# Kernel optimization log

Hardware: AMD Instinct MI355X
Metric: run time of the kernel (lower is better)

The kernel has to match this reference:

```python
import jax, jax.numpy as jnp
import numpy as np

B, N, S, DG, C_IN, C_OUT, HID = 2, 128, 4, 8, 4, 8, 32


def setup_inputs() -> dict:
    key = jax.random.key(0)
    ks = jax.random.split(key, 10)

    def w(k, shape, fan_in):
        return jax.random.normal(k, shape, jnp.float32) / np.float32(np.sqrt(fan_in))

    return {
        "pairwise_g": jax.random.normal(ks[0], (B, N, N, S, S, DG), jnp.float32),
        "coset_functions": jax.random.normal(ks[1], (B, N, S, C_IN), jnp.float32),
        "mask": jax.random.bernoulli(ks[2], 0.9, (B, N, S)),
        "ky_W1": w(ks[3], (C_IN, HID, 2), 2), "ky_b1": jnp.zeros((C_IN, HID), jnp.float32),
        "ky_W2": w(ks[4], (C_IN, HID, HID), HID), "ky_b2": jnp.zeros((C_IN, HID), jnp.float32),
        "ky_W3": w(ks[5], (C_IN, 1, HID), HID), "ky_b3": jnp.zeros((C_IN, 1), jnp.float32),
        "kg_W1": w(ks[6], (C_IN, HID, DG), DG), "kg_b1": jnp.zeros((C_IN, HID), jnp.float32),
        "kg_W2": w(ks[7], (C_IN, HID, HID), HID), "kg_b2": jnp.zeros((C_IN, HID), jnp.float32),
        "kg_W3": w(ks[8], (C_IN, 1, HID), HID), "kg_b3": jnp.zeros((C_IN, 1), jnp.float32),
        "w_out": w(ks[9], (C_OUT, C_IN), C_IN),
    }


def _mlp(x, W1, b1, W2, b2, W3, b3):
    # NerualNetKernel with bn=False, act=Swish: (Linear + SiLU) x 3, incl. output layer.
    h = jax.nn.silu(x @ W1.T + b1)
    h = jax.nn.silu(h @ W2.T + b2)
    return jax.nn.silu(h @ W3.T + b3)


def reference(pairwise_g, coset_functions, mask,
              ky_W1, ky_b1, ky_W2, ky_b2, ky_W3, ky_b3,
              kg_W1, kg_b1, kg_W2, kg_b2, kg_W3, kg_b3, w_out):
    b, n, _, s, _, _ = pairwise_g.shape
    c_in = coset_functions.shape[-1]
    key_mask = mask[:, None, :, None, :, None]  # (B,1,N,1,S,1) masks key points/samples
    outs = []
    for i in range(c_in):  # fixed small channel loop, as in the original module
        f = coset_functions[..., i:i + 1]  # (B,N,S,1)
        y1 = jnp.broadcast_to(f[:, None, :, None, :, :], (b, n, n, s, s, 1))  # key side
        y2 = jnp.broadcast_to(f[:, :, None, :, None, :], (b, n, n, s, s, 1))  # query side
        y = jnp.concatenate([y1, y2], axis=-1)  # (B,N,N,S,S,2)
        k = (_mlp(y, ky_W1[i], ky_b1[i], ky_W2[i], ky_b2[i], ky_W3[i], ky_b3[i])
             + _mlp(pairwise_g, kg_W1[i], kg_b1[i], kg_W2[i], kg_b2[i], kg_W3[i], kg_b3[i]))
        att = jnp.where(key_mask, jnp.exp(k), jnp.zeros((), k.dtype))  # (B,N,N,S,S,1)
        att = att / att.sum(axis=(2, 4), keepdims=True)
        f = f + (att * f[:, None, :, None, :, :]).sum(axis=(2, 4))  # residual + weighted agg
        outs.append(f)
    cf = jnp.concatenate(outs, axis=-1)  # (B,N,S,C_IN)
    cf = cf * mask[..., None].astype(cf.dtype)
    return cf @ w_out.T  # (B,N,S,C_OUT), bias-free output transform
```

## Files before the change

kernel.cpp:

```cpp
#include <hip/hip_runtime.h>
#include <hip/hip_bf16.h>

#define BB   2
#define NN   128
#define SS   4
#define DGG  8
#define CIN  4
#define COUT 8
#define HH   32
#define NT   256

typedef __attribute__((ext_vector_type(4))) float          fvec4;
typedef __attribute__((ext_vector_type(4))) unsigned short usvec4;
typedef __attribute__((ext_vector_type(8))) unsigned short usvec8;
typedef __attribute__((ext_vector_type(2))) __fp16         half2v;
typedef __attribute__((ext_vector_type(8))) __fp16         f16x8;
typedef __attribute__((ext_vector_type(4))) float          f32x4;
typedef __attribute__((ext_vector_type(4))) unsigned int   uvec4;

__device__ __forceinline__ float bf2f(unsigned short u) {
    return __uint_as_float(((unsigned int)u) << 16);
}
__device__ __forceinline__ float silu_f(float x) {
    float e = __builtin_amdgcn_exp2f(x * -1.44269504f);
    return x * __builtin_amdgcn_rcpf(1.0f + e);
}
__device__ __forceinline__ float exp_f(float x) {
    return __builtin_amdgcn_exp2f(x * 1.44269504f);
}

__device__ __forceinline__ unsigned int pk2u(float a, float b) {
#if __has_builtin(__builtin_amdgcn_cvt_pkrtz)
    half2v h = __builtin_amdgcn_cvt_pkrtz(a, b);
#else
    half2v h; h[0] = (__fp16)a; h[1] = (__fp16)b;
#endif
    union { half2v h; unsigned int u; } x; x.h = h; return x.u;
}
union FU { uvec4 u; f16x8 h; };
__device__ __forceinline__ f16x8 mk_frag(unsigned a, unsigned b, unsigned c, unsigned d) {
    FU x; x.u = (uvec4){a, b, c, d}; return x.h;
}
__device__ __forceinline__ f16x8 mk_fragv(uvec4 u) {
    FU x; x.u = u; return x.h;
}
__device__ __forceinline__ f16x8 silu_frag(f32x4 a, f32x4 b) {
    return mk_frag(pk2u(silu_f(a[0]), silu_f(a[1])),
                   pk2u(silu_f(a[2]), silu_f(a[3])),
                   pk2u(silu_f(b[0]), silu_f(b[1])),
                   pk2u(silu_f(b[2]), silu_f(b[3])));
}

__device__ __forceinline__ float loadS(const void* p, int idx, int fmode) {
    return fmode ? bf2f(((const unsigned short*)p)[idx])
                 : ((const float*)p)[idx];
}
__device__ __forceinline__ void load8(const void* p, int base, int fmode, float* dst) {
    if (fmode) {
        usvec8 v = *(const usvec8*)((const unsigned short*)p + base);
#pragma unroll
        for (int d = 0; d < 8; ++d) dst[d] = bf2f(v[d]);
    } else {
        fvec4 a = *(const fvec4*)((const float*)p + base);
        fvec4 b = *(const fvec4*)((const float*)p + base + 4);
        dst[0] = a[0]; dst[1] = a[1]; dst[2] = a[2]; dst[3] = a[3];
        dst[4] = b[0]; dst[5] = b[1]; dst[6] = b[2]; dst[7] = b[3];
    }
}
__device__ __forceinline__ int load_mask(const void* p, int idx, int mmode) {
    if (mmode == 0) return ((const int*)p)[idx] != 0;
    if (mmode == 1) return ((const unsigned short*)p)[idx] != 0;
    if (mmode == 2) return ((const unsigned char*)p)[idx] != 0;
    return ((const unsigned int*)p)[idx] != 0;
}
__device__ __forceinline__ void stage_pk(unsigned int* dst, const void* src,
                                         int pairs, int fmode, int tid) {
    if (fmode) {
        const unsigned short* s = (const unsigned short*)src;
        for (int x = tid; x < pairs; x += NT)
            dst[x] = pk2u(bf2f(s[2 * x]), bf2f(s[2 * x + 1]));
    } else {
        const float* s = (const float*)src;
        for (int x = tid; x < pairs; x += NT)
            dst[x] = pk2u(s[2 * x], s[2 * x + 1]);
    }
}
__device__ __forceinline__ void copy_arr(float* sm, const void* src, int off,
                                         int cnt, int fmode, int tid) {
    if (fmode) {
        const unsigned short* s = (const unsigned short*)src;
        for (int x = tid; x < cnt; x += NT) sm[off + x] = bf2f(s[x]);
    } else {
        const float* s = (const float*)src;
        for (int x = tid; x < cnt; x += NT) sm[off + x] = s[x];
    }
}
__device__ __forceinline__ void detect_inline(const void* g_mask, const void* g_coset,
                                              int tid, int* smi, int slot) {
    if (tid < 64) {
        const unsigned short* cu = (const unsigned short*)g_coset;
        unsigned short v = cu[2 * tid];
        int e = (v >> 7) & 0xFF;
        int hits = __popcll(__ballot(e >= 110 && e <= 135));
        int fmode_ = (hits > 32) ? 1 : 0;
        const unsigned short* mu = (const unsigned short*)g_mask;
        int evenBF = 0, any3 = 0, anyByte = 0;
        for (int r = 0; r < 8; ++r) {
            int idx = tid + r * 64;
            unsigned short m = mu[idx];
            if (m == 0x3F80) { any3 = 1; if (!(idx & 1)) evenBF = 1; }
            if (m == 0x0101 || m == 0x0100) anyByte = 1;
        }
        evenBF  = (__ballot(evenBF)  != 0ull);
        any3    = (__ballot(any3)    != 0ull);
        anyByte = (__ballot(anyByte) != 0ull);
        if (tid == 0) {
            smi[slot]     = fmode_;
            smi[slot + 1] = evenBF ? 1 : (any3 ? 3 : (anyByte ? 2 : 0));
        }
    }
}

#define UG_G    0
#define F_FA    2048
#define U_YW1n  4096
#define U_GW1   4608
#define U_GB1q  5120
#define U_W2Y   5632
#define U_W2G   7680
#define F_YB2   9728
#define F_GB2   9856
#define U_YW3   9984
#define U_GW3   10048
#define F_YB3   10112
#define F_GB3   10116
#define U_CB1   10120
#define F_RED   10128
#define F_MODE  10160
#define U_TOTAL 10162

__global__ __launch_bounds__(NT, 4) void emha_mfma(
    const void* __restrict__ g_pw, const void* __restrict__ g_coset,
    const void* __restrict__ g_mask,
    const void* yW1, const void* yb1, const void* yW2, const void* yb2,
    const void* yW3, const void* yb3,
    const void* gW1, const void* gb1, const void* gW2, const void* gb2,
    const void* gW3, const void* gb3,
    const void* wout, void* outp)
{
    __shared__ __align__(16) unsigned int smu[U_TOTAL];
    float* smf = (float*)smu;
    int*   smi = (int*)smu;
    const int tid = threadIdx.x;

    detect_inline(g_mask, g_coset, tid, smi, F_MODE);
    __syncthreads();
    const int fmode = smi[F_MODE];
    const int mmode = smi[F_MODE + 1];
    __syncthreads();

    const int bn = blockIdx.x >> 2;
    const int s1 = blockIdx.x & 3;
    const int b  = bn >> 7;
    const int n1 = bn & 127;

#pragma unroll
    for (int it = 0; it < 2; ++it) {
        const int pos = tid + it * 256;
        const int n2 = pos >> 2, s2 = pos & 3;
        float g8[8];
        load8(g_pw, (((bn * NN + n2) * SS + s1) * SS + s2) * DGG, fmode, g8);
#pragma unroll
        for (int q = 0; q < 4; ++q)
            smu[UG_G + pos * 4 + q] = pk2u(g8[2 * q], g8[2 * q + 1]);
    }
    for (int x = tid; x < 2048; x += NT)
        smf[F_FA + x] = loadS(g_coset, b * 2048 + x, fmode);
    for (int x = tid; x < 128; x += NT) {
        smu[U_YW1n + x * 4 + 0] = pk2u(loadS(yW1, 2 * x, fmode), loadS(yW1, 2 * x + 1, fmode));
        smu[U_YW1n + x * 4 + 1] = pk2u(loadS(yb1, x, fmode), 0.f);
        smu[U_YW1n + x * 4 + 2] = 0u;
        smu[U_YW1n + x * 4 + 3] = 0u;
        smu[U_GB1q + x * 4 + 0] = pk2u(loadS(gb1, x, fmode), 0.f);
        smu[U_GB1q + x * 4 + 1] = 0u;
        smu[U_GB1q + x * 4 + 2] = 0u;
        smu[U_GB1q + x * 4 + 3] = 0u;
    }
    stage_pk(&smu[U_GW1], gW1, 512,  fmode, tid);
    stage_pk(&smu[U_W2Y], yW2, 2048, fmode, tid);
    stage_pk(&smu[U_W2G], gW2, 2048, fmode, tid);
    stage_pk(&smu[U_YW3], yW3, 64,   fmode, tid);
    stage_pk(&smu[U_GW3], gW3, 64,   fmode, tid);
    copy_arr(smf, yb2, F_YB2, 128, fmode, tid);
    copy_arr(smf, gb2, F_GB2, 128, fmode, tid);
    copy_arr(smf, yb3, F_YB3, 4, fmode, tid);
    copy_arr(smf, gb3, F_GB3, 4, fmode, tid);
    if (tid < 8) smu[U_CB1 + tid] = (tid == 0) ? 0x00003C00u : 0u;

    const int lane = tid & 63;
    const int wave = tid >> 6;
    const int mLo = load_mask(g_mask, b * 512 + wave * 128 + lane, mmode);
    const int mHi = load_mask(g_mask, b * 512 + wave * 128 + 64 + lane, mmode);
    const unsigned long long kmL = __ballot(mLo != 0);
    const unsigned long long kmH = __ballot(mHi != 0);
    __syncthreads();

    const int quad = lane >> 4;
    const int col  = lane & 15;
    const int qpos = n1 * 4 + s1;
    const int h0   = ((col >> 2) << 3) + (col & 3);
    const unsigned* Zp = &smu[U_CB1 + 4];
    const f32x4 zf = {0.f, 0.f, 0.f, 0.f};

#pragma unroll 1
    for (int ci = 0; ci < CIN; ++ci) {
        const int rowy = (ci * 32 + h0) * 4;
        const f16x8 AY1a = mk_fragv(*(const uvec4*)((quad == 0) ? &smu[U_YW1n + rowy] : Zp));
        const f16x8 AY1b = mk_fragv(*(const uvec4*)((quad == 0) ? &smu[U_YW1n + rowy + 16] : Zp));
        const f16x8 GA = mk_fragv(*(const uvec4*)((quad == 0) ? &smu[U_GW1 + rowy]
                                   : (quad == 1) ? &smu[U_GB1q + rowy] : Zp));
        const f16x8 GB = mk_fragv(*(const uvec4*)((quad == 0) ? &smu[U_GW1 + rowy + 16]
                                   : (quad == 1) ? &smu[U_GB1q + rowy + 16] : Zp));
        const f16x8 Ay0 = mk_fragv(*(const uvec4*)&smu[U_W2Y + ci * 512 + h0 * 16 + quad * 4]);
        const f16x8 Ay1 = mk_fragv(*(const uvec4*)&smu[U_W2Y + ci * 512 + (h0 + 4) * 16 + quad * 4]);
        const f16x8 Ag0 = mk_fragv(*(const uvec4*)&smu[U_W2G + ci * 512 + h0 * 16 + quad * 4]);
        const f16x8 Ag1 = mk_fragv(*(const uvec4*)&smu[U_W2G + ci * 512 + (h0 + 4) * 16 + quad * 4]);
        const fvec4 cY0 = *(const fvec4*)&smf[F_YB2 + ci * 32 + quad * 8];
        const fvec4 cY1 = *(const fvec4*)&smf[F_YB2 + ci * 32 + quad * 8 + 4];
        const fvec4 cG0 = *(const fvec4*)&smf[F_GB2 + ci * 32 + quad * 8];
        const fvec4 cG1 = *(const fvec4*)&smf[F_GB2 + ci * 32 + quad * 8 + 4];
        const f16x8 A3y = mk_fragv(*(const uvec4*)((col == 0) ? &smu[U_YW3 + ci * 16 + quad * 4] : Zp));
        const f16x8 A3g = mk_fragv(*(const uvec4*)((col == 0) ? &smu[U_GW3 + ci * 16 + quad * 4] : Zp));

        const float fb  = smf[F_FA + qpos * 4 + ci];
        const float b3y = smf[F_YB3 + ci];
        const float b3g = smf[F_GB3 + ci];

        const unsigned* pBg = (quad == 0) ? &smu[UG_G + (wave * 128 + col) * 4]
                            : ((quad == 1) ? &smu[U_CB1] : Zp);
        const int stepBg = (quad == 0) ? 64 : 0;
        const float* pFA = &smf[F_FA + (wave * 128 + col) * 4 + ci];

        float aN = 0.f, aD = 0.f;
#pragma unroll 2
        for (int t = 0; t < 8; ++t) {
            const uvec4 gq = *(const uvec4*)pBg;
            const float fap = *pFA;
            const f16x8 Bg1 = mk_fragv(gq);
            const f16x8 B1y = mk_frag(pk2u(fap, fb), 0x00003C00u, 0u, 0u);

            f32x4 d1a, d1b, dga, dgb, dy0, dy1, dg0, dg1, dy3, dg3;
#if defined(__HIP_DEVICE_COMPILE__)
            d1a = __builtin_amdgcn_mfma_f32_16x16x32_f16(AY1a, B1y, zf, 0, 0, 0);
            d1b = __builtin_amdgcn_mfma_f32_16x16x32_f16(AY1b, B1y, zf, 0, 0, 0);
            dga = __builtin_amdgcn_mfma_f32_16x16x32_f16(GA,   Bg1, zf, 0, 0, 0);
            dgb = __builtin_amdgcn_mfma_f32_16x16x32_f16(GB,   Bg1, zf, 0, 0, 0);
#else
            d1a = zf; d1b = zf; dga = zf; dgb = zf;
#endif
            const f16x8 By = silu_frag(d1a, d1b);
            const f16x8 Bg = silu_frag(dga, dgb);

#if defined(__HIP_DEVICE_COMPILE__)
            dy0 = __builtin_amdgcn_mfma_f32_16x16x32_f16(Ay0, By, cY0, 0, 0, 0);
            dy1 = __builtin_amdgcn_mfma_f32_16x16x32_f16(Ay1, By, cY1, 0, 0, 0);
            dg0 = __builtin_amdgcn_mfma_f32_16x16x32_f16(Ag0, Bg, cG0, 0, 0, 0);
            dg1 = __builtin_amdgcn_mfma_f32_16x16x32_f16(Ag1, Bg, cG1, 0, 0, 0);
#else
            dy0 = cY0; dy1 = cY1; dg0 = cG0; dg1 = cG1;
#endif
            const f16x8 By2 = silu_frag(dy0, dy1);
            const f16x8 Bg2 = silu_frag(dg0, dg1);

#if defined(__HIP_DEVICE_COMPILE__)
            dy3 = __builtin_amdgcn_mfma_f32_16x16x32_f16(A3y, By2, zf, 0, 0, 0);
            dg3 = __builtin_amdgcn_mfma_f32_16x16x32_f16(A3g, Bg2, zf, 0, 0, 0);
#else
            dy3 = zf; dg3 = zf;
#endif
            const float kyv = silu_f(dy3[0] + b3y);
            const float kgv = silu_f(dg3[0] + b3g);
            const unsigned long long sel = (t < 4) ? kmL : kmH;
            const int kb = (int)((sel >> (((t & 3) << 4) + col)) & 1);
            const float e = kb ? exp_f(kyv + kgv) : 0.f;
            aD += e;
            aN += e * fap;

            pBg += stepBg;
            pFA += 64;
        }
        aN += __shfl_xor(aN, 1);  aD += __shfl_xor(aD, 1);
        aN += __shfl_xor(aN, 2);  aD += __shfl_xor(aD, 2);
        aN += __shfl_xor(aN, 4);  aD += __shfl_xor(aD, 4);
        aN += __shfl_xor(aN, 8);  aD += __shfl_xor(aD, 8);
        if (lane == 0) {
            smf[F_RED + (wave * 4 + ci) * 2 + 0] = aN;
            smf[F_RED + (wave * 4 + ci) * 2 + 1] = aD;
        }
    }
    __syncthreads();

    if (tid < COUT) {
        const int o = tid;
        const int m1 = load_mask(g_mask, b * 512 + qpos, mmode);
        float acc = 0.f;
#pragma unroll
        for (int ci = 0; ci < CIN; ++ci) {
            float N = 0.f, D = 0.f;
#pragma unroll
            for (int w = 0; w < 4; ++w) {
                N += smf[F_RED + (w * 4 + ci) * 2 + 0];
                D += smf[F_RED + (w * 4 + ci) * 2 + 1];
            }
            const float fbv = smf[F_FA + qpos * 4 + ci];
            const float cf = m1 ? (fbv + N / D) : 0.f;
            acc += cf * loadS(wout, o * CIN + ci, fmode);
        }
        const int oidx = (bn * SS + s1) * COUT + o;
        if (fmode) ((__hip_bfloat16*)outp)[oidx] = __float2bfloat16(acc);
        else       ((float*)outp)[oidx] = acc;
    }
}

extern "C" void kernel_launch(void* const* d_in, const int* in_sizes, int n_in,
                              void* d_out, int out_size, void* d_ws, size_t ws_size,
                              hipStream_t stream) {
    emha_mfma<<<BB * NN * SS, NT, 0, stream>>>(
        d_in[0], d_in[1], d_in[2],
        d_in[3], d_in[4], d_in[5], d_in[6], d_in[7], d_in[8],
        d_in[9], d_in[10], d_in[11], d_in[12], d_in[13], d_in[14],
        d_in[15], d_out);
}
```

Measured before the change: 168.9 us.

## Use six waves per block with strided tile assignment and smem mask bytes

Raises the block from 4 to 6 waves and distributes the 32 key tiles round-robin across waves (6 iterations with a bounds check) instead of a fixed 8 tiles per wave. The key mask is staged into shared memory as bytes, replacing per-wave ballots, and the layer-1 weight buffers are compacted so zero fragments are built in registers instead of read from padded LDS. The intent is more latency hiding per CU from extra waves. The cost is load imbalance (two waves do 6 tiles, four do 5), a divergent branch inside the loop, and a larger block that may cut blocks per CU.

Measured after the change: 208.7 us. +23.5%, slower.

```diff
diff --git a/kernel.cpp b/kernel.cpp
--- a/kernel.cpp
+++ b/kernel.cpp
@@ -8,7 +8,8 @@
 #define CIN  4
 #define COUT 8
 #define HH   32
-#define NT   256
+#define NT   384
+#define NW   6
 
 typedef __attribute__((ext_vector_type(4))) float          fvec4;
 typedef __attribute__((ext_vector_type(4))) unsigned short usvec4;
@@ -123,23 +124,24 @@
 
 #define UG_G    0
 #define F_FA    2048
-#define U_YW1n  4096
-#define U_GW1   4608
-#define U_GB1q  5120
-#define U_W2Y   5632
-#define U_W2G   7680
-#define F_YB2   9728
-#define F_GB2   9856
-#define U_YW3   9984
-#define U_GW3   10048
-#define F_YB3   10112
-#define F_GB3   10116
-#define U_CB1   10120
-#define F_RED   10128
-#define F_MODE  10160
-#define U_TOTAL 10162
-
-__global__ __launch_bounds__(NT, 4) void emha_mfma(
+#define U_MASKB 4096
+#define U_YW1c  4224
+#define U_GW1   4480
+#define U_GB1c  4992
+#define U_W2Y   5120
+#define U_W2G   7168
+#define F_YB2   9216
+#define F_GB2   9344
+#define U_YW3   9472
+#define U_GW3   9536
+#define F_YB3   9600
+#define F_GB3   9604
+#define U_CB1   9608
+#define F_RED   9616
+#define F_MODE  9664
+#define U_TOTAL 9666
+
+__global__ __launch_bounds__(NT, NW) void emha_mfma(
     const void* __restrict__ g_pw, const void* __restrict__ g_coset,
     const void* __restrict__ g_mask,
     const void* yW1, const void* yb1, const void* yW2, const void* yb2,
@@ -164,9 +166,7 @@
     const int b  = bn >> 7;
     const int n1 = bn & 127;
 
-#pragma unroll
-    for (int it = 0; it < 2; ++it) {
-        const int pos = tid + it * 256;
+    for (int pos = tid; pos < 512; pos += NT) {
         const int n2 = pos >> 2, s2 = pos & 3;
         float g8[8];
         load8(g_pw, (((bn * NN + n2) * SS + s1) * SS + s2) * DGG, fmode, g8);
@@ -176,15 +176,15 @@
     }
     for (int x = tid; x < 2048; x += NT)
         smf[F_FA + x] = loadS(g_coset, b * 2048 + x, fmode);
+    {
+        unsigned char* mbs = (unsigned char*)&smu[U_MASKB];
+        for (int x = tid; x < 512; x += NT)
+            mbs[x] = (unsigned char)load_mask(g_mask, b * 512 + x, mmode);
+    }
     for (int x = tid; x < 128; x += NT) {
-        smu[U_YW1n + x * 4 + 0] = pk2u(loadS(yW1, 2 * x, fmode), loadS(yW1, 2 * x + 1, fmode));
-        smu[U_YW1n + x * 4 + 1] = pk2u(loadS(yb1, x, fmode), 0.f);
-        smu[U_YW1n + x * 4 + 2] = 0u;
-        smu[U_YW1n + x * 4 + 3] = 0u;
-        smu[U_GB1q + x * 4 + 0] = pk2u(loadS(gb1, x, fmode), 0.f);
-        smu[U_GB1q + x * 4 + 1] = 0u;
-        smu[U_GB1q + x * 4 + 2] = 0u;
-        smu[U_GB1q + x * 4 + 3] = 0u;
+        smu[U_YW1c + x * 2 + 0] = pk2u(loadS(yW1, 2 * x, fmode), loadS(yW1, 2 * x + 1, fmode));
+        smu[U_YW1c + x * 2 + 1] = pk2u(loadS(yb1, x, fmode), 0.f);
+        smu[U_GB1c + x]         = pk2u(loadS(gb1, x, fmode), 0.f);
     }
     stage_pk(&smu[U_GW1], gW1, 512,  fmode, tid);
     stage_pk(&smu[U_W2Y], yW2, 2048, fmode, tid);
@@ -196,31 +196,35 @@
     copy_arr(smf, yb3, F_YB3, 4, fmode, tid);
     copy_arr(smf, gb3, F_GB3, 4, fmode, tid);
     if (tid < 8) smu[U_CB1 + tid] = (tid == 0) ? 0x00003C00u : 0u;
+    __syncthreads();
 
     const int lane = tid & 63;
     const int wave = tid >> 6;
-    const int mLo = load_mask(g_mask, b * 512 + wave * 128 + lane, mmode);
-    const int mHi = load_mask(g_mask, b * 512 + wave * 128 + 64 + lane, mmode);
-    const unsigned long long kmL = __ballot(mLo != 0);
-    const unsigned long long kmH = __ballot(mHi != 0);
-    __syncthreads();
-
     const int quad = lane >> 4;
     const int col  = lane & 15;
     const int qpos = n1 * 4 + s1;
     const int h0   = ((col >> 2) << 3) + (col & 3);
-    const unsigned* Zp = &smu[U_CB1 + 4];
+    const unsigned char* mb = (const unsigned char*)&smu[U_MASKB];
     const f32x4 zf = {0.f, 0.f, 0.f, 0.f};
+    const uvec4 zz = {0u, 0u, 0u, 0u};
 
 #pragma unroll 1
     for (int ci = 0; ci < CIN; ++ci) {
-        const int rowy = (ci * 32 + h0) * 4;
-        const f16x8 AY1a = mk_fragv(*(const uvec4*)((quad == 0) ? &smu[U_YW1n + rowy] : Zp));
-        const f16x8 AY1b = mk_fragv(*(const uvec4*)((quad == 0) ? &smu[U_YW1n + rowy + 16] : Zp));
-        const f16x8 GA = mk_fragv(*(const uvec4*)((quad == 0) ? &smu[U_GW1 + rowy]
-                                   : (quad == 1) ? &smu[U_GB1q + rowy] : Zp));
-        const f16x8 GB = mk_fragv(*(const uvec4*)((quad == 0) ? &smu[U_GW1 + rowy + 16]
-                                   : (quad == 1) ? &smu[U_GB1q + rowy + 16] : Zp));
+        const int rw = ci * 32 + h0;
+        uvec4 va = zz, vb = zz, ga = zz, gb = zz;
+        if (quad == 0) {
+            va[0] = smu[U_YW1c + rw * 2];       va[1] = smu[U_YW1c + rw * 2 + 1];
+            vb[0] = smu[U_YW1c + (rw + 4) * 2]; vb[1] = smu[U_YW1c + (rw + 4) * 2 + 1];
+            ga = *(const uvec4*)&smu[U_GW1 + rw * 4];
+            gb = *(const uvec4*)&smu[U_GW1 + (rw + 4) * 4];
+        } else if (quad == 1) {
+            ga[0] = smu[U_GB1c + rw];
+            gb[0] = smu[U_GB1c + rw + 4];
+        }
+        const f16x8 AY1a = mk_fragv(va);
+        const f16x8 AY1b = mk_fragv(vb);
+        const f16x8 GA   = mk_fragv(ga);
+        const f16x8 GB   = mk_fragv(gb);
         const f16x8 Ay0 = mk_fragv(*(const uvec4*)&smu[U_W2Y + ci * 512 + h0 * 16 + quad * 4]);
         const f16x8 Ay1 = mk_fragv(*(const uvec4*)&smu[U_W2Y + ci * 512 + (h0 + 4) * 16 + quad * 4]);
         const f16x8 Ag0 = mk_fragv(*(const uvec4*)&smu[U_W2G + ci * 512 + h0 * 16 + quad * 4]);
@@ -229,65 +233,62 @@
         const fvec4 cY1 = *(const fvec4*)&smf[F_YB2 + ci * 32 + quad * 8 + 4];
         const fvec4 cG0 = *(const fvec4*)&smf[F_GB2 + ci * 32 + quad * 8];
         const fvec4 cG1 = *(const fvec4*)&smf[F_GB2 + ci * 32 + quad * 8 + 4];
-        const f16x8 A3y = mk_fragv(*(const uvec4*)((col == 0) ? &smu[U_YW3 + ci * 16 + quad * 4] : Zp));
-        const f16x8 A3g = mk_fragv(*(const uvec4*)((col == 0) ? &smu[U_GW3 + ci * 16 + quad * 4] : Zp));
+        const f16x8 A3y = mk_fragv((col == 0) ? *(const uvec4*)&smu[U_YW3 + ci * 16 + quad * 4] : zz);
+        const f16x8 A3g = mk_fragv((col == 0) ? *(const uvec4*)&smu[U_GW3 + ci * 16 + quad * 4] : zz);
 
         const float fb  = smf[F_FA + qpos * 4 + ci];
         const float b3y = smf[F_YB3 + ci];
         const float b3g = smf[F_GB3 + ci];
 
-        const unsigned* pBg = (quad == 0) ? &smu[UG_G + (wave * 128 + col) * 4]
-                            : ((quad == 1) ? &smu[U_CB1] : Zp);
-        const int stepBg = (quad == 0) ? 64 : 0;
-        const float* pFA = &smf[F_FA + (wave * 128 + col) * 4 + ci];
-
         float aN = 0.f, aD = 0.f;
-#pragma unroll 2
-        for (int t = 0; t < 8; ++t) {
-            const uvec4 gq = *(const uvec4*)pBg;
-            const float fap = *pFA;
-            const f16x8 Bg1 = mk_fragv(gq);
-            const f16x8 B1y = mk_frag(pk2u(fap, fb), 0x00003C00u, 0u, 0u);
-
-            f32x4 d1a, d1b, dga, dgb, dy0, dy1, dg0, dg1, dy3, dg3;
+#pragma unroll 1
+        for (int t = 0; t < 6; ++t) {
+            const int tile = t * NW + wave;
+            if (tile < 32) {
+                const int pos = tile * 16 + col;
+                const float fap = smf[F_FA + pos * 4 + ci];
+                const int km = mb[pos];
+                uvec4 gq;
+                if (quad == 0) gq = *(const uvec4*)&smu[UG_G + pos * 4];
+                else           gq = (uvec4){(quad == 1) ? 0x00003C00u : 0u, 0u, 0u, 0u};
+                const f16x8 Bg1 = mk_fragv(gq);
+                const f16x8 B1y = mk_frag(pk2u(fap, fb), 0x00003C00u, 0u, 0u);
+
+                f32x4 d1a, d1b, dga, dgb, dy0, dy1, dg0, dg1, dy3, dg3;
 #if defined(__HIP_DEVICE_COMPILE__)
-            d1a = __builtin_amdgcn_mfma_f32_16x16x32_f16(AY1a, B1y, zf, 0, 0, 0);
-            d1b = __builtin_amdgcn_mfma_f32_16x16x32_f16(AY1b, B1y, zf, 0, 0, 0);
-            dga = __builtin_amdgcn_mfma_f32_16x16x32_f16(GA,   Bg1, zf, 0, 0, 0);
-            dgb = __builtin_amdgcn_mfma_f32_16x16x32_f16(GB,   Bg1, zf, 0, 0, 0);
+                d1a = __builtin_amdgcn_mfma_f32_16x16x32_f16(AY1a, B1y, zf, 0, 0, 0);
+                d1b = __builtin_amdgcn_mfma_f32_16x16x32_f16(AY1b, B1y, zf, 0, 0, 0);
+                dga = __builtin_amdgcn_mfma_f32_16x16x32_f16(GA,   Bg1, zf, 0, 0, 0);
+                dgb = __builtin_amdgcn_mfma_f32_16x16x32_f16(GB,   Bg1, zf, 0, 0, 0);
 #else
-            d1a = zf; d1b = zf; dga = zf; dgb = zf;
+                d1a = zf; d1b = zf; dga = zf; dgb = zf;
 #endif
-            const f16x8 By = silu_frag(d1a, d1b);
-            const f16x8 Bg = silu_frag(dga, dgb);
+                const f16x8 By = silu_frag(d1a, d1b);
+                const f16x8 Bg = silu_frag(dga, dgb);
 
 #if defined(__HIP_DEVICE_COMPILE__)
-            dy0 = __builtin_amdgcn_mfma_f32_16x16x32_f16(Ay0, By, cY0, 0, 0, 0);
-            dy1 = __builtin_amdgcn_mfma_f32_16x16x32_f16(Ay1, By, cY1, 0, 0, 0);
-            dg0 = __builtin_amdgcn_mfma_f32_16x16x32_f16(Ag0, Bg, cG0, 0, 0, 0);
-            dg1 = __builtin_amdgcn_mfma_f32_16x16x32_f16(Ag1, Bg, cG1, 0, 0, 0);
+                dy0 = __builtin_amdgcn_mfma_f32_16x16x32_f16(Ay0, By, cY0, 0, 0, 0);
+                dy1 = __builtin_amdgcn_mfma_f32_16x16x32_f16(Ay1, By, cY1, 0, 0, 0);
+                dg0 = __builtin_amdgcn_mfma_f32_16x16x32_f16(Ag0, Bg, cG0, 0, 0, 0);
+                dg1 = __builtin_amdgcn_mfma_f32_16x16x32_f16(Ag1, Bg, cG1, 0, 0, 0);
 #else
-            dy0 = cY0; dy1 = cY1; dg0 = cG0; dg1 = cG1;
+                dy0 = cY0; dy1 = cY1; dg0 = cG0; dg1 = cG1;
 #endif
-            const f16x8 By2 = silu_frag(dy0, dy1);
-            const f16x8 Bg2 = silu_frag(dg0, dg1);
+                const f16x8 By2 = silu_frag(dy0, dy1);
+                const f16x8 Bg2 = silu_frag(dg0, dg1);
 
 #if defined(__HIP_DEVICE_COMPILE__)
-            dy3 = __builtin_amdgcn_mfma_f32_16x16x32_f16(A3y, By2, zf, 0, 0, 0);
-            dg3 = __builtin_amdgcn_mfma_f32_16x16x32_f16(A3g, Bg2, zf, 0, 0, 0);
+                dy3 = __builtin_amdgcn_mfma_f32_16x16x32_f16(A3y, By2, zf, 0, 0, 0);
+                dg3 = __builtin_amdgcn_mfma_f32_16x16x32_f16(A3g, Bg2, zf, 0, 0, 0);
 #else
-            dy3 = zf; dg3 = zf;
+                dy3 = zf; dg3 = zf;
 #endif
-            const float kyv = silu_f(dy3[0] + b3y);
-            const float kgv = silu_f(dg3[0] + b3g);
-            const unsigned long long sel = (t < 4) ? kmL : kmH;
-            const int kb = (int)((sel >> (((t & 3) << 4) + col)) & 1);
-            const float e = kb ? exp_f(kyv + kgv) : 0.f;
-            aD += e;
-            aN += e * fap;
-
-            pBg += stepBg;
-            pFA += 64;
+                const float kyv = silu_f(dy3[0] + b3y);
+                const float kgv = silu_f(dg3[0] + b3g);
+                const float e = km ? exp_f(kyv + kgv) : 0.f;
+                aD += e;
+                aN += e * fap;
+            }
         }
         aN += __shfl_xor(aN, 1);  aD += __shfl_xor(aD, 1);
         aN += __shfl_xor(aN, 2);  aD += __shfl_xor(aD, 2);
@@ -308,7 +309,7 @@
         for (int ci = 0; ci < CIN; ++ci) {
             float N = 0.f, D = 0.f;
 #pragma unroll
-            for (int w = 0; w < 4; ++w) {
+            for (int w = 0; w < NW; ++w) {
                 N += smf[F_RED + (w * 4 + ci) * 2 + 0];
                 D += smf[F_RED + (w * 4 + ci) * 2 + 1];
             }
```
